# Kernel optimization log

Hardware: AMD Instinct MI355X
Metric: run time of the kernel (lower is better)

The kernel has to match this reference:

```python
import jax, jax.numpy as jnp
import numpy as np

DIM = 1024
MLP_MULT = 4
NUM_EXPERTS = 8
EXPERT_HIDDEN = MLP_MULT * DIM // NUM_EXPERTS  # 512


def setup_inputs() -> dict:
    key = jax.random.key(0)
    k_x, k_r, k_fc, k_pj = jax.random.split(key, 4)
    x = jax.random.normal(k_x, (4, 4096, DIM), dtype=jnp.float32)
    # router: nn.Linear(dim, num_experts, bias=False) -> weight [E, D]
    w_router = jax.random.normal(k_r, (NUM_EXPERTS, DIM), dtype=jnp.float32) * (1.0 / np.sqrt(DIM))
    # per-expert fc: Linear(dim, hidden) weight [H, D]; stacked [E, H, D]
    w_fc = jax.random.normal(k_fc, (NUM_EXPERTS, EXPERT_HIDDEN, DIM), dtype=jnp.float32) * (1.0 / np.sqrt(DIM))
    # per-expert proj: Linear(hidden, dim) weight [D, H]; stacked [E, D, H]
    # (_zero_init in the original; use small random values so the reference output is non-trivial)
    w_proj = jax.random.normal(k_pj, (NUM_EXPERTS, DIM, EXPERT_HIDDEN), dtype=jnp.float32) * (1.0 / np.sqrt(EXPERT_HIDDEN))
    return {"x": x, "w_router": w_router, "w_fc": w_fc, "w_proj": w_proj}


def reference(x, w_router, w_fc, w_proj):
    # Router on detached input; top-1 expert per token.
    logits = jnp.einsum('bsd,ed->bse', jax.lax.stop_gradient(x), w_router)
    weights = jax.nn.softmax(logits, axis=-1)  # computed as in original (unused in output)
    indices = jnp.argmax(weights, axis=-1)     # [B, S]
    onehot = jax.nn.one_hot(indices, NUM_EXPERTS, dtype=x.dtype)  # [B, S, E]
    # Dense dispatch: run all experts, combine with one-hot (equivalent to mask gather/scatter).
    h = jnp.einsum('bsd,ehd->bseh', x, w_fc)              # [B, S, E, H]
    h = jnp.where(h >= 0, h, 0.5 * h)                      # leaky_relu(negative_slope=0.5)
    h = h * h                                              # square
    out = jnp.einsum('bseh,edh,bse->bsd', h, w_proj, onehot)
    return out
```

## Files before the change

### kernel.cpp

```cpp
#include <hip/hip_runtime.h>
#include <stdint.h>
#include <stddef.h>

#define DIM 1024
#define NEXP 8
#define HID 512
#define NTOK 16384
#define NB_HIST 64
#define NB_ROUTER 1024
#define NB_CAST 512

typedef __attribute__((ext_vector_type(4))) float f32x4;
typedef __attribute__((ext_vector_type(8))) short short8;
typedef __attribute__((ext_vector_type(4))) unsigned short u16x4;
typedef __attribute__((ext_vector_type(8))) unsigned short u16x8;

__device__ __forceinline__ unsigned short f2b(float f) {
  unsigned int u = __float_as_uint(f);
  return (unsigned short)((u + 0x7FFFu + ((u >> 16) & 1u)) >> 16);
}

__device__ __forceinline__ void gload_lds16(const unsigned short* g, unsigned short* l) {
  __builtin_amdgcn_global_load_lds((const __attribute__((address_space(1))) void*)g,
                                   (__attribute__((address_space(3))) void*)l, 16, 0, 0);
}

__global__ __launch_bounds__(256) void k_router_cast(
    const float* __restrict__ x, const float* __restrict__ wr,
    int* __restrict__ eid,
    const float* __restrict__ wfc, const float* __restrict__ wpj,
    unsigned short* __restrict__ oa, unsigned short* __restrict__ ob) {
  int bid = blockIdx.x;
  if (bid < NB_ROUTER) {
    int w = threadIdx.x >> 6, lane = threadIdx.x & 63;
    int t0 = bid * 16 + w * 4;
    const float* xr = x + (size_t)t0 * DIM;
    float s[4][NEXP];
#pragma unroll
    for (int j = 0; j < 4; j++)
#pragma unroll
      for (int e = 0; e < NEXP; e++) s[j][e] = 0.f;
#pragma unroll
    for (int i = 0; i < 4; i++) {
      f32x4 xv[4];
#pragma unroll
      for (int j = 0; j < 4; j++) xv[j] = *(const f32x4*)(xr + j * DIM + lane * 4 + 256 * i);
#pragma unroll
      for (int e = 0; e < NEXP; e++) {
        f32x4 wv = *(const f32x4*)(wr + e * DIM + lane * 4 + 256 * i);
#pragma unroll
        for (int j = 0; j < 4; j++)
          s[j][e] += xv[j].x * wv.x + xv[j].y * wv.y + xv[j].z * wv.z + xv[j].w * wv.w;
      }
    }
#pragma unroll
    for (int j = 0; j < 4; j++)
#pragma unroll
      for (int e = 0; e < NEXP; e++) {
        float v = s[j][e];
#pragma unroll
        for (int off = 32; off > 0; off >>= 1) v += __shfl_xor(v, off);
        s[j][e] = v;
      }
    if (lane == 0) {
#pragma unroll
      for (int j = 0; j < 4; j++) {
        int be = 0;
        float bv = s[j][0];
#pragma unroll
        for (int e = 1; e < NEXP; e++) {
          if (s[j][e] > bv) { bv = s[j][e]; be = e; }
        }
        eid[t0 + j] = be;
      }
    }
  } else {
    const int n4 = NEXP * HID * DIM / 4;
    int stride = NB_CAST * 256;
    for (int i = (bid - NB_ROUTER) * 256 + (int)threadIdx.x; i < n4; i += stride) {
      f32x4 va = ((const f32x4*)wfc)[i];
      f32x4 vb = ((const f32x4*)wpj)[i];
      u16x4 ua, ub;
      ua.x = f2b(va.x); ua.y = f2b(va.y); ua.z = f2b(va.z); ua.w = f2b(va.w);
      ub.x = f2b(vb.x); ub.y = f2b(vb.y); ub.z = f2b(vb.z); ub.w = f2b(vb.w);
      ((u16x4*)oa)[i] = ua;
      ((u16x4*)ob)[i] = ub;
    }
  }
}

__global__ __launch_bounds__(256) void k_hist(const int* __restrict__ eid,
                                              int* __restrict__ bc) {
  __shared__ int h[NEXP];
  if (threadIdx.x < NEXP) h[threadIdx.x] = 0;
  __syncthreads();
  int tok = blockIdx.x * (NTOK / NB_HIST) + threadIdx.x;
  atomicAdd(&h[eid[tok]], 1);
  __syncthreads();
  if (threadIdx.x < NEXP) bc[blockIdx.x * NEXP + threadIdx.x] = h[threadIdx.x];
}

__global__ void k_scan(const int* __restrict__ bc, int* __restrict__ offs,
                       int* __restrict__ base) {
  __shared__ int cnt[NEXP];
  __shared__ int so[NEXP + 1];
  int t = threadIdx.x;
  if (t < NEXP) {
    int run = 0;
    for (int b = 0; b < NB_HIST; b++) {
      base[b * NEXP + t] = run;
      run += bc[b * NEXP + t];
    }
    cnt[t] = run;
  }
  __syncthreads();
  if (t == 0) {
    int a = 0;
    for (int e = 0; e < NEXP; e++) { so[e] = a; a += cnt[e]; }
    so[NEXP] = a;
  }
  __syncthreads();
  if (t < NEXP + 1) offs[t] = so[t];
  for (int i = t; i < NB_HIST * NEXP; i += blockDim.x) base[i] += so[i % NEXP];
}

__global__ __launch_bounds__(256) void k_scatter(const int* __restrict__ eid,
                                                 const int* __restrict__ base,
                                                 int* __restrict__ tlist) {
  __shared__ int cur[NEXP];
  if (threadIdx.x < NEXP) cur[threadIdx.x] = base[blockIdx.x * NEXP + threadIdx.x];
  __syncthreads();
  int tok = blockIdx.x * (NTOK / NB_HIST) + threadIdx.x;
  int e = eid[tok];
  int pos = atomicAdd(&cur[e], 1);
  tlist[pos] = tok;
}

__device__ __forceinline__ bool tile_map(const int* offs, int NB, int& e, int& mb,
                                         int& nb) {
  int l = ((int)blockIdx.x & 7) * ((int)gridDim.x >> 3) + ((int)blockIdx.x >> 3);
  e = -1; mb = 0; nb = 0;
  int acc2 = 0;
#pragma unroll
  for (int i = 0; i < NEXP; i++) {
    int mi = offs[i + 1] - offs[i];
    int tb = ((mi + 127) >> 7) * NB;
    if (e < 0 && l < acc2 + tb) {
      int r = l - acc2;
      e = i; mb = r / NB; nb = r % NB;
    }
    acc2 += tb;
  }
  return e >= 0;
}

__global__ __launch_bounds__(256) void k_gemm_fc(
    const float* __restrict__ x, const unsigned short* __restrict__ wb,
    const int* __restrict__ offs, const int* __restrict__ tlist,
    unsigned short* __restrict__ hout) {
  constexpr int KDIM = DIM, NDIM = HID;
  int e, mb, nb;
  if (!tile_map(offs, 4, e, mb, nb)) return;
  int off = offs[e], me = offs[e + 1] - off, m0 = mb * 128, n0 = nb * 128;

  __shared__ unsigned short As[3][128 * 32];
  __shared__ unsigned short Bs[3][128 * 32];

  int t = threadIdx.x, lane = t & 63, w = t >> 6;
  int wm = w >> 1, wn = w & 1;

  int kb = (lane & 3) ^ ((lane >> 3) & 3);

  const unsigned short* bsrc[2];
  const float* af32[2];
#pragma unroll
  for (int i = 0; i < 2; i++) {
    int r = i * 64 + w * 16 + (lane >> 2);
    bsrc[i] = wb + ((size_t)e * NDIM + n0 + r) * (size_t)KDIM + kb * 8;
    int gm = m0 + r;
    if (gm > me - 1) gm = me - 1;
    af32[i] = x + (size_t)tlist[off + gm] * DIM + kb * 8;
  }
  int awoff0 = (w * 16) * 32 + lane * 8;
  int awoff1 = (64 + w * 16) * 32 + lane * 8;

  f32x4 acc[4][4] = {};
  constexpr int NT = KDIM / 32;

  unsigned short* a0 = &As[0][0]; unsigned short* b0 = &Bs[0][0];
  unsigned short* a1 = &As[1][0]; unsigned short* b1 = &Bs[1][0];
  unsigned short* a2 = &As[2][0]; unsigned short* b2 = &Bs[2][0];

  f32x4 r00, r01, r10, r11;

#define ISSUE_A(kt_)                                              \
  do {                                                            \
    r00 = *(const f32x4*)(af32[0] + (kt_) * 32);                  \
    r01 = *(const f32x4*)(af32[0] + (kt_) * 32 + 4);              \
    r10 = *(const f32x4*)(af32[1] + (kt_) * 32);                  \
    r11 = *(const f32x4*)(af32[1] + (kt_) * 32 + 4);              \
  } while (0)
#define ISSUE_B(kt_, db_)                                         \
  do {                                                            \
    gload_lds16(bsrc[0] + (kt_) * 32, (db_) + (w * 16) * 32);     \
    gload_lds16(bsrc[1] + (kt_) * 32, (db_) + (64 + w * 16) * 32);\
  } while (0)
#define WRITE_A(da_)                                              \
  do {                                                            \
    u16x8 c0, c1;                                                 \
    c0[0] = f2b(r00.x); c0[1] = f2b(r00.y); c0[2] = f2b(r00.z); c0[3] = f2b(r00.w); \
    c0[4] = f2b(r01.x); c0[5] = f2b(r01.y); c0[6] = f2b(r01.z); c0[7] = f2b(r01.w); \
    c1[0] = f2b(r10.x); c1[1] = f2b(r10.y); c1[2] = f2b(r10.z); c1[3] = f2b(r10.w); \
    c1[4] = f2b(r11.x); c1[5] = f2b(r11.y); c1[6] = f2b(r11.z); c1[7] = f2b(r11.w); \
    *(u16x8*)&(da_)[awoff0] = c0;                                 \
    *(u16x8*)&(da_)[awoff1] = c1;                                 \
  } while (0)

  ISSUE_A(0);
  ISSUE_B(0, b0);
  ISSUE_B(1, b1);

  for (int kt = 0; kt < NT; kt++) {
    if (kt == NT - 1) {
      asm volatile("s_waitcnt vmcnt(0)" ::: "memory");
    } else {
      asm volatile("s_waitcnt vmcnt(2)" ::: "memory");
    }
    __builtin_amdgcn_sched_barrier(0);
    WRITE_A(a0);
    asm volatile("s_waitcnt lgkmcnt(0)" ::: "memory");
    __builtin_amdgcn_sched_barrier(0);
    __builtin_amdgcn_s_barrier();
    if (kt + 1 < NT) ISSUE_A(kt + 1);
    if (kt + 2 < NT) ISSUE_B(kt + 2, b2);

    short8 af[4], bf[4];
#pragma unroll
    for (int i = 0; i < 4; i++) {
      int ra = wm * 64 + i * 16 + (lane & 15);
      int ca = (lane >> 4) ^ ((ra >> 1) & 3);
      af[i] = *(const short8*)&a0[ra * 32 + ca * 8];
      int rbb = wn * 64 + i * 16 + (lane & 15);
      int cb = (lane >> 4) ^ ((rbb >> 1) & 3);
      bf[i] = *(const short8*)&b0[rbb * 32 + cb * 8];
    }
    __builtin_amdgcn_s_setprio(1);
#pragma unroll
    for (int mi = 0; mi < 4; mi++)
#pragma unroll
      for (int ni = 0; ni < 4; ni++)
        acc[mi][ni] =
            __builtin_amdgcn_mfma_f32_16x16x32_bf16(af[mi], bf[ni], acc[mi][ni], 0, 0, 0);
    __builtin_amdgcn_s_setprio(0);

    unsigned short* ta = a0; a0 = a1; a1 = a2; a2 = ta;
    unsigned short* tb = b0; b0 = b1; b1 = b2; b2 = tb;
  }
#undef ISSUE_A
#undef ISSUE_B
#undef WRITE_A

  int rb = (lane >> 4) * 4, cb = lane & 15;
#pragma unroll
  for (int mi = 0; mi < 4; mi++) {
#pragma unroll
    for (int j = 0; j < 4; j++) {
      int ml = wm * 64 + mi * 16 + rb + j;
      if (m0 + ml < me) {
#pragma unroll
        for (int ni = 0; ni < 4; ni++) {
          int col = n0 + wn * 64 + ni * 16 + cb;
          float v = acc[mi][ni][j];
          v = (v >= 0.f) ? v * v : 0.25f * v * v;
          hout[(size_t)(off + m0 + ml) * HID + col] = f2b(v);
        }
      }
    }
  }
}

__global__ __launch_bounds__(256) void k_gemm_pj(
    const unsigned short* __restrict__ hin, const unsigned short* __restrict__ wb,
    const int* __restrict__ offs, const int* __restrict__ tlist,
    float* __restrict__ out) {
  constexpr int KDIM = HID, NDIM = DIM;
  int e, mb, nb;
  if (!tile_map(offs, 8, e, mb, nb)) return;
  int off = offs[e], me = offs[e + 1] - off, m0 = mb * 128, n0 = nb * 128;

  __shared__ unsigned short lds[3][2][128 * 32];

  int t = threadIdx.x, lane = t & 63, w = t >> 6;
  int wm = w >> 1, wn = w & 1;

  int kb = (lane & 3) ^ ((lane >> 3) & 3);

  const unsigned short* asrc[2];
  const unsigned short* bsrc[2];
#pragma unroll
  for (int i = 0; i < 2; i++) {
    int r = i * 64 + w * 16 + (lane >> 2);
    int gm = m0 + r;
    if (gm > me - 1) gm = me - 1;
    asrc[i] = hin + (size_t)(off + gm) * KDIM + kb * 8;
    bsrc[i] = wb + ((size_t)e * NDIM + n0 + r) * (size_t)KDIM + kb * 8;
  }

  f32x4 acc[4][4] = {};
  constexpr int NT = KDIM / 32;

  unsigned short* b0a = &lds[0][0][0]; unsigned short* b0b = &lds[0][1][0];
  unsigned short* b1a = &lds[1][0][0]; unsigned short* b1b = &lds[1][1][0];
  unsigned short* b2a = &lds[2][0][0]; unsigned short* b2b = &lds[2][1][0];

#define STAGE(kt_, da_, db_)                                       \
  do {                                                             \
    gload_lds16(asrc[0] + (kt_) * 32, (da_) + (w * 16) * 32);      \
    gload_lds16(asrc[1] + (kt_) * 32, (da_) + (64 + w * 16) * 32); \
    gload_lds16(bsrc[0] + (kt_) * 32, (db_) + (w * 16) * 32);      \
    gload_lds16(bsrc[1] + (kt_) * 32, (db_) + (64 + w * 16) * 32); \
  } while (0)

  STAGE(0, b0a, b0b);
  STAGE(1, b1a, b1b);

  for (int kt = 0; kt < NT; kt++) {
    if (kt < NT - 1) {
      asm volatile("s_waitcnt vmcnt(4)" ::: "memory");
    } else {
      asm volatile("s_waitcnt vmcnt(0)" ::: "memory");
    }
    __builtin_amdgcn_s_barrier();

    if (kt + 2 < NT) STAGE(kt + 2, b2a, b2b);

    short8 af[4], bf[4];
#pragma unroll
    for (int i = 0; i < 4; i++) {
      int ra = wm * 64 + i * 16 + (lane & 15);
      int ca = (lane >> 4) ^ ((ra >> 1) & 3);
      af[i] = *(const short8*)&b0a[ra * 32 + ca * 8];
      int rbb = wn * 64 + i * 16 + (lane & 15);
      int cb = (lane >> 4) ^ ((rbb >> 1) & 3);
      bf[i] = *(const short8*)&b0b[rbb * 32 + cb * 8];
    }
    __builtin_amdgcn_s_setprio(1);
#pragma unroll
    for (int mi = 0; mi < 4; mi++)
#pragma unroll
      for (int ni = 0; ni < 4; ni++)
        acc[mi][ni] =
            __builtin_amdgcn_mfma_f32_16x16x32_bf16(af[mi], bf[ni], acc[mi][ni], 0, 0, 0);
    __builtin_amdgcn_s_setprio(0);

    unsigned short* ta = b0a; b0a = b1a; b1a = b2a; b2a = ta;
    unsigned short* tb = b0b; b0b = b1b; b1b = b2b; b2b = tb;
  }
#undef STAGE

  int rb = (lane >> 4) * 4, cb = lane & 15;
#pragma unroll
  for (int mi = 0; mi < 4; mi++) {
#pragma unroll
    for (int j = 0; j < 4; j++) {
      int ml = wm * 64 + mi * 16 + rb + j;
      if (m0 + ml < me) {
        int tok = tlist[off + m0 + ml];
#pragma unroll
        for (int ni = 0; ni < 4; ni++) {
          int col = n0 + wn * 64 + ni * 16 + cb;
          out[(size_t)tok * DIM + col] = acc[mi][ni][j];
        }
      }
    }
  }
}

extern "C" void kernel_launch(void* const* d_in, const int* in_sizes, int n_in,
                              void* d_out, int out_size, void* d_ws, size_t ws_size,
                              hipStream_t stream) {
  const float* x = (const float*)d_in[0];
  const float* wr = (const float*)d_in[1];
  const float* wfc = (const float*)d_in[2];
  const float* wpj = (const float*)d_in[3];
  float* out = (float*)d_out;

  uintptr_t p = (uintptr_t)d_ws;
  int* offs = (int*)p;  p += 256;
  int* bc = (int*)p;    p += sizeof(int) * NB_HIST * NEXP;
  int* base = (int*)p;  p += sizeof(int) * NB_HIST * NEXP;
  int* eid = (int*)p;   p += sizeof(int) * NTOK;
  int* tlist = (int*)p; p += sizeof(int) * NTOK;
  unsigned short* wfc_b = (unsigned short*)p; p += (size_t)NEXP * HID * DIM * 2;
  unsigned short* wpj_b = (unsigned short*)p; p += (size_t)NEXP * DIM * HID * 2;
  unsigned short* hbuf = (unsigned short*)p;  p += (size_t)NTOK * HID * 2;

  k_router_cast<<<NB_ROUTER + NB_CAST, 256, 0, stream>>>(
      x, wr, eid, wfc, wpj, wfc_b, wpj_b);
  k_hist<<<NB_HIST, 256, 0, stream>>>(eid, bc);
  k_scan<<<1, 256, 0, stream>>>(bc, offs, base);
  k_scatter<<<NB_HIST, 256, 0, stream>>>(eid, base, tlist);
  k_gemm_fc<<<dim3(544), 256, 0, stream>>>(x, wfc_b, offs, tlist, hbuf);
  k_gemm_pj<<<dim3(1080), 256, 0, stream>>>(hbuf, wpj_b, offs, tlist, out);
}
```

Before: 107.4 us.

## Restructure fc GEMM pipeline to prefetch A two stages ahead with register double-buffering

The fc GEMM main loop now issues fp32 activation loads two k-steps ahead into alternating register sets and converts/writes them to LDS after the MFMA block rather than before it. The A LDS buffer drops from three stages to two, and the loop is unrolled by two so the register sets swap statically. The intent is to hide global load latency of the gathered fp32 rows behind MFMA work and cut one barrier-bound stall per iteration. In exchange it uses more VGPRs for the extra prefetch registers and depends on hand-tuned vmcnt counts being correct.

```diff
diff --git a/kernel.cpp b/kernel.cpp
--- a/kernel.cpp
+++ b/kernel.cpp
@@ -163,7 +163,7 @@
   if (!tile_map(offs, 4, e, mb, nb)) return;
   int off = offs[e], me = offs[e + 1] - off, m0 = mb * 128, n0 = nb * 128;
 
-  __shared__ unsigned short As[3][128 * 32];
+  __shared__ unsigned short As[2][128 * 32];
   __shared__ unsigned short Bs[3][128 * 32];
 
   int t = threadIdx.x, lane = t & 63, w = t >> 6;
@@ -187,78 +187,93 @@
   f32x4 acc[4][4] = {};
   constexpr int NT = KDIM / 32;
 
-  unsigned short* a0 = &As[0][0]; unsigned short* b0 = &Bs[0][0];
-  unsigned short* a1 = &As[1][0]; unsigned short* b1 = &Bs[1][0];
-  unsigned short* a2 = &As[2][0]; unsigned short* b2 = &Bs[2][0];
-
-  f32x4 r00, r01, r10, r11;
-
-#define ISSUE_A(kt_)                                              \
-  do {                                                            \
-    r00 = *(const f32x4*)(af32[0] + (kt_) * 32);                  \
-    r01 = *(const f32x4*)(af32[0] + (kt_) * 32 + 4);              \
-    r10 = *(const f32x4*)(af32[1] + (kt_) * 32);                  \
-    r11 = *(const f32x4*)(af32[1] + (kt_) * 32 + 4);              \
+  unsigned short* aS0 = &As[0][0];
+  unsigned short* aS1 = &As[1][0];
+  unsigned short* b0c = &Bs[0][0];
+  unsigned short* b1c = &Bs[1][0];
+  unsigned short* b2c = &Bs[2][0];
+
+  f32x4 p0, p1, p2, p3;
+  f32x4 q0, q1, q2, q3;
+
+#define ISSUE_A(kt_, R0, R1, R2, R3)                  \
+  do {                                                \
+    R0 = *(const f32x4*)(af32[0] + (kt_) * 32);       \
+    R1 = *(const f32x4*)(af32[0] + (kt_) * 32 + 4);   \
+    R2 = *(const f32x4*)(af32[1] + (kt_) * 32);       \
+    R3 = *(const f32x4*)(af32[1] + (kt_) * 32 + 4);   \
   } while (0)
-#define ISSUE_B(kt_, db_)                                         \
-  do {                                                            \
-    gload_lds16(bsrc[0] + (kt_) * 32, (db_) + (w * 16) * 32);     \
-    gload_lds16(bsrc[1] + (kt_) * 32, (db_) + (64 + w * 16) * 32);\
+#define ISSUE_B(kt_, db_)                                          \
+  do {                                                             \
+    gload_lds16(bsrc[0] + (kt_) * 32, (db_) + (w * 16) * 32);      \
+    gload_lds16(bsrc[1] + (kt_) * 32, (db_) + (64 + w * 16) * 32); \
   } while (0)
-#define WRITE_A(da_)                                              \
-  do {                                                            \
-    u16x8 c0, c1;                                                 \
-    c0[0] = f2b(r00.x); c0[1] = f2b(r00.y); c0[2] = f2b(r00.z); c0[3] = f2b(r00.w); \
-    c0[4] = f2b(r01.x); c0[5] = f2b(r01.y); c0[6] = f2b(r01.z); c0[7] = f2b(r01.w); \
-    c1[0] = f2b(r10.x); c1[1] = f2b(r10.y); c1[2] = f2b(r10.z); c1[3] = f2b(r10.w); \
-    c1[4] = f2b(r11.x); c1[5] = f2b(r11.y); c1[6] = f2b(r11.z); c1[7] = f2b(r11.w); \
-    *(u16x8*)&(da_)[awoff0] = c0;                                 \
-    *(u16x8*)&(da_)[awoff1] = c1;                                 \
+#define WRITE_A(da_, R0, R1, R2, R3)                                                \
+  do {                                                                              \
+    u16x8 c0, c1;                                                                   \
+    c0[0] = f2b(R0.x); c0[1] = f2b(R0.y); c0[2] = f2b(R0.z); c0[3] = f2b(R0.w);     \
+    c0[4] = f2b(R1.x); c0[5] = f2b(R1.y); c0[6] = f2b(R1.z); c0[7] = f2b(R1.w);     \
+    c1[0] = f2b(R2.x); c1[1] = f2b(R2.y); c1[2] = f2b(R2.z); c1[3] = f2b(R2.w);     \
+    c1[4] = f2b(R3.x); c1[5] = f2b(R3.y); c1[6] = f2b(R3.z); c1[7] = f2b(R3.w);     \
+    *(u16x8*)&(da_)[awoff0] = c0;                                                   \
+    *(u16x8*)&(da_)[awoff1] = c1;                                                   \
   } while (0)
 
-  ISSUE_A(0);
-  ISSUE_B(0, b0);
-  ISSUE_B(1, b1);
-
-  for (int kt = 0; kt < NT; kt++) {
-    if (kt == NT - 1) {
-      asm volatile("s_waitcnt vmcnt(0)" ::: "memory");
-    } else {
-      asm volatile("s_waitcnt vmcnt(2)" ::: "memory");
-    }
-    __builtin_amdgcn_sched_barrier(0);
-    WRITE_A(a0);
-    asm volatile("s_waitcnt lgkmcnt(0)" ::: "memory");
-    __builtin_amdgcn_sched_barrier(0);
-    __builtin_amdgcn_s_barrier();
-    if (kt + 1 < NT) ISSUE_A(kt + 1);
-    if (kt + 2 < NT) ISSUE_B(kt + 2, b2);
-
-    short8 af[4], bf[4];
-#pragma unroll
-    for (int i = 0; i < 4; i++) {
-      int ra = wm * 64 + i * 16 + (lane & 15);
-      int ca = (lane >> 4) ^ ((ra >> 1) & 3);
-      af[i] = *(const short8*)&a0[ra * 32 + ca * 8];
-      int rbb = wn * 64 + i * 16 + (lane & 15);
-      int cb = (lane >> 4) ^ ((rbb >> 1) & 3);
-      bf[i] = *(const short8*)&b0[rbb * 32 + cb * 8];
-    }
-    __builtin_amdgcn_s_setprio(1);
-#pragma unroll
-    for (int mi = 0; mi < 4; mi++)
-#pragma unroll
-      for (int ni = 0; ni < 4; ni++)
-        acc[mi][ni] =
-            __builtin_amdgcn_mfma_f32_16x16x32_bf16(af[mi], bf[ni], acc[mi][ni], 0, 0, 0);
-    __builtin_amdgcn_s_setprio(0);
-
-    unsigned short* ta = a0; a0 = a1; a1 = a2; a2 = ta;
-    unsigned short* tb = b0; b0 = b1; b1 = b2; b2 = tb;
+#define FC_BODY(k_, AR_, AW_, I0, I1, I2, I3, W0, W1, W2, W3)                   \
+  do {                                                                          \
+    if ((k_) + 2 < NT) {                                                        \
+      ISSUE_A((k_) + 2, I0, I1, I2, I3);                                        \
+      ISSUE_B((k_) + 2, b2c);                                                   \
+    }                                                                           \
+    short8 af[4], bf[4];                                                        \
+    _Pragma("unroll") for (int i = 0; i < 4; i++) {                             \
+      int ra = wm * 64 + i * 16 + (lane & 15);                                  \
+      int ca = (lane >> 4) ^ ((ra >> 1) & 3);                                   \
+      af[i] = *(const short8*)&(AR_)[ra * 32 + ca * 8];                         \
+      int rbb = wn * 64 + i * 16 + (lane & 15);                                 \
+      int cb2 = (lane >> 4) ^ ((rbb >> 1) & 3);                                 \
+      bf[i] = *(const short8*)&b0c[rbb * 32 + cb2 * 8];                         \
+    }                                                                           \
+    __builtin_amdgcn_s_setprio(1);                                              \
+    _Pragma("unroll") for (int mi = 0; mi < 4; mi++)                            \
+      _Pragma("unroll") for (int ni = 0; ni < 4; ni++)                          \
+        acc[mi][ni] = __builtin_amdgcn_mfma_f32_16x16x32_bf16(                  \
+            af[mi], bf[ni], acc[mi][ni], 0, 0, 0);                              \
+    __builtin_amdgcn_s_setprio(0);                                              \
+    if ((k_) + 1 < NT) {                                                        \
+      if ((k_) + 2 < NT)                                                        \
+        asm volatile("s_waitcnt vmcnt(8)" ::: "memory");                        \
+      else                                                                      \
+        asm volatile("s_waitcnt vmcnt(2)" ::: "memory");                        \
+      WRITE_A(AW_, W0, W1, W2, W3);                                             \
+      if ((k_) + 2 < NT)                                                        \
+        asm volatile("s_waitcnt vmcnt(6)" ::: "memory");                        \
+      else                                                                      \
+        asm volatile("s_waitcnt vmcnt(0)" ::: "memory");                        \
+      asm volatile("s_waitcnt lgkmcnt(0)" ::: "memory");                        \
+      __builtin_amdgcn_s_barrier();                                             \
+    }                                                                           \
+    unsigned short* tmpb_ = b0c; b0c = b1c; b1c = b2c; b2c = tmpb_;             \
+  } while (0)
+
+  ISSUE_A(0, p0, p1, p2, p3);
+  ISSUE_B(0, b0c);
+  ISSUE_A(1, q0, q1, q2, q3);
+  ISSUE_B(1, b1c);
+  asm volatile("s_waitcnt vmcnt(8)" ::: "memory");
+  WRITE_A(aS0, p0, p1, p2, p3);
+  asm volatile("s_waitcnt vmcnt(6)" ::: "memory");
+  asm volatile("s_waitcnt lgkmcnt(0)" ::: "memory");
+  __builtin_amdgcn_s_barrier();
+
+  for (int kt = 0; kt < NT; kt += 2) {
+    FC_BODY(kt,     aS0, aS1, p0, p1, p2, p3, q0, q1, q2, q3);
+    FC_BODY(kt + 1, aS1, aS0, q0, q1, q2, q3, p0, p1, p2, p3);
   }
 #undef ISSUE_A
 #undef ISSUE_B
 #undef WRITE_A
+#undef FC_BODY
 
   int rb = (lane >> 4) * 4, cb = lane & 15;
 #pragma unroll
```

After: 127.5 us. 18.8% more time.

## Widen proj GEMM tile to 128x256 and use packed bf16 conversion

Applied to the files above, without the earlier changes.

The projection GEMM now computes 128x256 output tiles instead of 128x128. Each wave holds a 64x128 accumulator and the grid is halved. This cuts redundant reloads of the A operand (the hidden activations) and doubles the MFMA work done per staged tile. Separately, the scalar bf16 rounding in the weight cast and in the fc A-tile write is replaced by the hardware v_cvt_pk_bf16_f32 instruction, which reduces ALU work. The larger tile raises register pressure (128 accumulator floats) and LDS use, and with fewer blocks there may be more load imbalance across experts.

```diff
diff --git a/kernel.cpp b/kernel.cpp
--- a/kernel.cpp
+++ b/kernel.cpp
@@ -14,10 +14,18 @@
 typedef __attribute__((ext_vector_type(8))) short short8;
 typedef __attribute__((ext_vector_type(4))) unsigned short u16x4;
 typedef __attribute__((ext_vector_type(8))) unsigned short u16x8;
+typedef __attribute__((ext_vector_type(2))) unsigned int u32x2;
+typedef __attribute__((ext_vector_type(4))) unsigned int u32x4;
 
 __device__ __forceinline__ unsigned short f2b(float f) {
   unsigned int u = __float_as_uint(f);
   return (unsigned short)((u + 0x7FFFu + ((u >> 16) & 1u)) >> 16);
+}
+
+__device__ __forceinline__ unsigned int pk_bf16(float a, float b) {
+  unsigned int r;
+  asm volatile("v_cvt_pk_bf16_f32 %0, %1, %2" : "=v"(r) : "v"(a), "v"(b));
+  return r;
 }
 
 __device__ __forceinline__ void gload_lds16(const unsigned short* g, unsigned short* l) {
@@ -80,11 +88,11 @@
     for (int i = (bid - NB_ROUTER) * 256 + (int)threadIdx.x; i < n4; i += stride) {
       f32x4 va = ((const f32x4*)wfc)[i];
       f32x4 vb = ((const f32x4*)wpj)[i];
-      u16x4 ua, ub;
-      ua.x = f2b(va.x); ua.y = f2b(va.y); ua.z = f2b(va.z); ua.w = f2b(va.w);
-      ub.x = f2b(vb.x); ub.y = f2b(vb.y); ub.z = f2b(vb.z); ub.w = f2b(vb.w);
-      ((u16x4*)oa)[i] = ua;
-      ((u16x4*)ob)[i] = ub;
+      u32x2 ua, ub;
+      ua.x = pk_bf16(va.x, va.y); ua.y = pk_bf16(va.z, va.w);
+      ub.x = pk_bf16(vb.x, vb.y); ub.y = pk_bf16(vb.z, vb.w);
+      ((u32x2*)oa)[i] = ua;
+      ((u32x2*)ob)[i] = ub;
     }
   }
 }
@@ -207,13 +215,13 @@
   } while (0)
 #define WRITE_A(da_)                                              \
   do {                                                            \
-    u16x8 c0, c1;                                                 \
-    c0[0] = f2b(r00.x); c0[1] = f2b(r00.y); c0[2] = f2b(r00.z); c0[3] = f2b(r00.w); \
-    c0[4] = f2b(r01.x); c0[5] = f2b(r01.y); c0[6] = f2b(r01.z); c0[7] = f2b(r01.w); \
-    c1[0] = f2b(r10.x); c1[1] = f2b(r10.y); c1[2] = f2b(r10.z); c1[3] = f2b(r10.w); \
-    c1[4] = f2b(r11.x); c1[5] = f2b(r11.y); c1[6] = f2b(r11.z); c1[7] = f2b(r11.w); \
-    *(u16x8*)&(da_)[awoff0] = c0;                                 \
-    *(u16x8*)&(da_)[awoff1] = c1;                                 \
+    u32x4 c0, c1;                                                 \
+    c0.x = pk_bf16(r00.x, r00.y); c0.y = pk_bf16(r00.z, r00.w);   \
+    c0.z = pk_bf16(r01.x, r01.y); c0.w = pk_bf16(r01.z, r01.w);   \
+    c1.x = pk_bf16(r10.x, r10.y); c1.y = pk_bf16(r10.z, r10.w);   \
+    c1.z = pk_bf16(r11.x, r11.y); c1.w = pk_bf16(r11.z, r11.w);   \
+    *(u32x4*)&(da_)[awoff0] = c0;                                 \
+    *(u32x4*)&(da_)[awoff1] = c1;                                 \
   } while (0)
 
   ISSUE_A(0);
@@ -279,16 +287,17 @@
   }
 }
 
-__global__ __launch_bounds__(256) void k_gemm_pj(
+__global__ __launch_bounds__(256, 2) void k_gemm_pj(
     const unsigned short* __restrict__ hin, const unsigned short* __restrict__ wb,
     const int* __restrict__ offs, const int* __restrict__ tlist,
     float* __restrict__ out) {
   constexpr int KDIM = HID, NDIM = DIM;
   int e, mb, nb;
-  if (!tile_map(offs, 8, e, mb, nb)) return;
-  int off = offs[e], me = offs[e + 1] - off, m0 = mb * 128, n0 = nb * 128;
-
-  __shared__ unsigned short lds[3][2][128 * 32];
+  if (!tile_map(offs, 4, e, mb, nb)) return;
+  int off = offs[e], me = offs[e + 1] - off, m0 = mb * 128, n0 = nb * 256;
+
+  __shared__ unsigned short Asl[3][128 * 32];
+  __shared__ unsigned short Bsl[3][256 * 32];
 
   int t = threadIdx.x, lane = t & 63, w = t >> 6;
   int wm = w >> 1, wn = w & 1;
@@ -296,65 +305,74 @@
   int kb = (lane & 3) ^ ((lane >> 3) & 3);
 
   const unsigned short* asrc[2];
-  const unsigned short* bsrc[2];
+  const unsigned short* bsrc[4];
 #pragma unroll
   for (int i = 0; i < 2; i++) {
     int r = i * 64 + w * 16 + (lane >> 2);
     int gm = m0 + r;
     if (gm > me - 1) gm = me - 1;
     asrc[i] = hin + (size_t)(off + gm) * KDIM + kb * 8;
-    bsrc[i] = wb + ((size_t)e * NDIM + n0 + r) * (size_t)KDIM + kb * 8;
-  }
-
-  f32x4 acc[4][4] = {};
+  }
+#pragma unroll
+  for (int j = 0; j < 4; j++) {
+    int r = j * 64 + w * 16 + (lane >> 2);
+    bsrc[j] = wb + ((size_t)e * NDIM + n0 + r) * (size_t)KDIM + kb * 8;
+  }
+
+  f32x4 acc[4][8] = {};
   constexpr int NT = KDIM / 32;
 
-  unsigned short* b0a = &lds[0][0][0]; unsigned short* b0b = &lds[0][1][0];
-  unsigned short* b1a = &lds[1][0][0]; unsigned short* b1b = &lds[1][1][0];
-  unsigned short* b2a = &lds[2][0][0]; unsigned short* b2b = &lds[2][1][0];
-
-#define STAGE(kt_, da_, db_)                                       \
-  do {                                                             \
-    gload_lds16(asrc[0] + (kt_) * 32, (da_) + (w * 16) * 32);      \
-    gload_lds16(asrc[1] + (kt_) * 32, (da_) + (64 + w * 16) * 32); \
-    gload_lds16(bsrc[0] + (kt_) * 32, (db_) + (w * 16) * 32);      \
-    gload_lds16(bsrc[1] + (kt_) * 32, (db_) + (64 + w * 16) * 32); \
+  unsigned short* a0 = &Asl[0][0]; unsigned short* b0 = &Bsl[0][0];
+  unsigned short* a1 = &Asl[1][0]; unsigned short* b1 = &Bsl[1][0];
+  unsigned short* a2 = &Asl[2][0]; unsigned short* b2 = &Bsl[2][0];
+
+#define STAGE(kt_, da_, db_)                                           \
+  do {                                                                 \
+    gload_lds16(asrc[0] + (kt_) * 32, (da_) + (w * 16) * 32);          \
+    gload_lds16(asrc[1] + (kt_) * 32, (da_) + (64 + w * 16) * 32);     \
+    gload_lds16(bsrc[0] + (kt_) * 32, (db_) + (w * 16) * 32);          \
+    gload_lds16(bsrc[1] + (kt_) * 32, (db_) + (64 + w * 16) * 32);     \
+    gload_lds16(bsrc[2] + (kt_) * 32, (db_) + (128 + w * 16) * 32);    \
+    gload_lds16(bsrc[3] + (kt_) * 32, (db_) + (192 + w * 16) * 32);    \
   } while (0)
 
-  STAGE(0, b0a, b0b);
-  STAGE(1, b1a, b1b);
+  STAGE(0, a0, b0);
+  STAGE(1, a1, b1);
 
   for (int kt = 0; kt < NT; kt++) {
     if (kt < NT - 1) {
-      asm volatile("s_waitcnt vmcnt(4)" ::: "memory");
+      asm volatile("s_waitcnt vmcnt(6)" ::: "memory");
     } else {
       asm volatile("s_waitcnt vmcnt(0)" ::: "memory");
     }
     __builtin_amdgcn_s_barrier();
 
-    if (kt + 2 < NT) STAGE(kt + 2, b2a, b2b);
-
-    short8 af[4], bf[4];
+    if (kt + 2 < NT) STAGE(kt + 2, a2, b2);
+
+    short8 af[4], bf[8];
 #pragma unroll
     for (int i = 0; i < 4; i++) {
       int ra = wm * 64 + i * 16 + (lane & 15);
       int ca = (lane >> 4) ^ ((ra >> 1) & 3);
-      af[i] = *(const short8*)&b0a[ra * 32 + ca * 8];
-      int rbb = wn * 64 + i * 16 + (lane & 15);
+      af[i] = *(const short8*)&a0[ra * 32 + ca * 8];
+    }
+#pragma unroll
+    for (int i = 0; i < 8; i++) {
+      int rbb = wn * 128 + i * 16 + (lane & 15);
       int cb = (lane >> 4) ^ ((rbb >> 1) & 3);
-      bf[i] = *(const short8*)&b0b[rbb * 32 + cb * 8];
+      bf[i] = *(const short8*)&b0[rbb * 32 + cb * 8];
     }
     __builtin_amdgcn_s_setprio(1);
 #pragma unroll
     for (int mi = 0; mi < 4; mi++)
 #pragma unroll
-      for (int ni = 0; ni < 4; ni++)
+      for (int ni = 0; ni < 8; ni++)
         acc[mi][ni] =
             __builtin_amdgcn_mfma_f32_16x16x32_bf16(af[mi], bf[ni], acc[mi][ni], 0, 0, 0);
     __builtin_amdgcn_s_setprio(0);
 
-    unsigned short* ta = b0a; b0a = b1a; b1a = b2a; b2a = ta;
-    unsigned short* tb = b0b; b0b = b1b; b1b = b2b; b2b = tb;
+    unsigned short* ta = a0; a0 = a1; a1 = a2; a2 = ta;
+    unsigned short* tb = b0; b0 = b1; b1 = b2; b2 = tb;
   }
 #undef STAGE
 
@@ -367,8 +385,8 @@
       if (m0 + ml < me) {
         int tok = tlist[off + m0 + ml];
 #pragma unroll
-        for (int ni = 0; ni < 4; ni++) {
-          int col = n0 + wn * 64 + ni * 16 + cb;
+        for (int ni = 0; ni < 8; ni++) {
+          int col = n0 + wn * 128 + ni * 16 + cb;
           out[(size_t)tok * DIM + col] = acc[mi][ni][j];
         }
       }
@@ -401,5 +419,5 @@
   k_scan<<<1, 256, 0, stream>>>(bc, offs, base);
   k_scatter<<<NB_HIST, 256, 0, stream>>>(eid, base, tlist);
   k_gemm_fc<<<dim3(544), 256, 0, stream>>>(x, wfc_b, offs, tlist, hbuf);
-  k_gemm_pj<<<dim3(1080), 256, 0, stream>>>(hbuf, wpj_b, offs, tlist, out);
-}
+  k_gemm_pj<<<dim3(544), 256, 0, stream>>>(hbuf, wpj_b, offs, tlist, out);
+}
```

Measured after the change: 113.3 us. +5.5%, slower.
